# Performance work log

Measured on AMD Instinct MI355X. Metric: run time of the kernel, lower is better.

## Reference

```python
import jax, jax.numpy as jnp
import numpy as np

N = 4096
IN_F = 128
OUT_F = 128
H = 4
D = OUT_F // H  # head_out = 32
SLOPE = 0.2
LN_EPS = 1e-5


def setup_inputs() -> dict:
    key = jax.random.key(0)
    k_x, k_adj, k_W, k_a = jax.random.split(key, 4)
    x = jax.random.normal(k_x, (N, IN_F), dtype=jnp.float32)
    adjacency = jax.random.randint(k_adj, (N, N), 0, 2).astype(jnp.bool_)
    # xavier-uniform-ish init scales
    w_std = float(np.sqrt(2.0 / (IN_F + H * D)))
    a_std = float(np.sqrt(2.0 / (H + 2 * D)))
    W = jax.random.normal(k_W, (H * D, IN_F), dtype=jnp.float32) * w_std  # torch Linear weight layout
    a = jax.random.normal(k_a, (H, 2 * D), dtype=jnp.float32) * a_std
    ln_gamma = jnp.ones((OUT_F,), dtype=jnp.float32)
    ln_beta = jnp.zeros((OUT_F,), dtype=jnp.float32)
    return {"x": x, "adjacency": adjacency, "W": W, "a": a,
            "ln_gamma": ln_gamma, "ln_beta": ln_beta}


def reference(x, adjacency, W, a, ln_gamma, ln_beta):
    # Wx: (N, H, D)
    Wx = (x @ W.T).reshape(N, H, D)
    # e[i,j,h] = leaky_relu( <Wx[i,h], a[h,:D]> + <Wx[j,h], a[h,D:]> )
    # (exact factorization of the original cat([Wx_i, Wx_j]) * a sum)
    alpha_i = jnp.einsum('nhd,hd->nh', Wx, a[:, :D])  # source/i term
    alpha_j = jnp.einsum('nhd,hd->nh', Wx, a[:, D:])  # neighbor/j term
    e = alpha_i[:, None, :] + alpha_j[None, :, :]      # (N, N, H)
    e = jnp.where(e >= 0, e, SLOPE * e)                # LeakyReLU
    e = jnp.where(adjacency[:, :, None], e, -jnp.inf)  # mask non-edges
    attn = jax.nn.softmax(e, axis=1)                   # softmax over j
    out = jnp.einsum('ijh,jhd->ihd', attn, Wx).reshape(N, H * D)
    y = out + x                                        # residual (dims match)
    mu = jnp.mean(y, axis=-1, keepdims=True)
    var = jnp.mean((y - mu) ** 2, axis=-1, keepdims=True)
    return ln_gamma * (y - mu) / jnp.sqrt(var + LN_EPS) + ln_beta
```

## Files before the change

### kernel.cpp

```cpp
#include <hip/hip_runtime.h>
#include <hip/hip_bf16.h>
#include <stdint.h>

#define NN 4096
#define SLOPE 0.2f
#define LOG2E 1.44269504088896340736f

typedef float f32x4 __attribute__((ext_vector_type(4)));
typedef short s16x8 __attribute__((ext_vector_type(8)));
typedef unsigned u32x4 __attribute__((ext_vector_type(4)));

static __device__ __forceinline__ unsigned f32_to_bf16_rne(float f) {
    unsigned u = __builtin_bit_cast(unsigned, f);
    return (u + 0x7FFFu + ((u >> 16) & 1u)) >> 16;
}

__global__ __launch_bounds__(256) void k01(const unsigned* __restrict__ adj_raw,
                                           const float* __restrict__ x,
                                           const float* __restrict__ W,
                                           const float* __restrict__ a,
                                           unsigned* __restrict__ bits,
                                           unsigned* __restrict__ wxb8,
                                           float* __restrict__ ai_s,
                                           float* __restrict__ ajT_s) {
    const int t = threadIdx.x;
    if (blockIdx.x < 2048) {
        __shared__ int s_i32;
        if (t == 0) {
            int all_small = 1;
            for (int i = 0; i < 32; ++i) all_small &= (adj_raw[i] <= 1u);
            s_i32 = all_small;
        }
        __syncthreads();
        const long o = (long)blockIdx.x * 256 + t;
        unsigned mm = 0;
        if (s_i32) {
            const u32x4* p = (const u32x4*)adj_raw + o * 8;
            #pragma unroll
            for (int g = 0; g < 8; ++g) {
                u32x4 v = p[g];
                mm |= (v.x & 1u) << (g * 4) | (v.y & 1u) << (g * 4 + 1) |
                      (v.z & 1u) << (g * 4 + 2) | (v.w & 1u) << (g * 4 + 3);
            }
        } else {
            const u32x4* p = (const u32x4*)adj_raw + o * 2;
            #pragma unroll
            for (int g = 0; g < 2; ++g) {
                u32x4 v = p[g];
                unsigned d[4] = {v.x, v.y, v.z, v.w};
                #pragma unroll
                for (int qq = 0; qq < 4; ++qq)
                    #pragma unroll
                    for (int b = 0; b < 4; ++b)
                        mm |= ((d[qq] >> (8 * b)) & 1u) << (g * 16 + qq * 4 + b);
            }
        }
        bits[o] = mm;
        return;
    }

    __shared__ unsigned short WL[128 * 136];
    __shared__ unsigned short XL[16 * 136];
    __shared__ float WxF[16 * 132];

    const int bid = blockIdx.x - 2048;
    const int i0 = bid * 16;

    for (int p4 = t; p4 < 4096; p4 += 256) {
        f32x4 w4 = *(const f32x4*)(W + 4 * p4);
        unsigned lo = f32_to_bf16_rne(w4.x) | (f32_to_bf16_rne(w4.y) << 16);
        unsigned hi = f32_to_bf16_rne(w4.z) | (f32_to_bf16_rne(w4.w) << 16);
        int c = (4 * p4) >> 7, k = (4 * p4) & 127;
        *(unsigned long long*)&WL[c * 136 + k] =
            (unsigned long long)lo | ((unsigned long long)hi << 32);
    }
    for (int p4 = t; p4 < 512; p4 += 256) {
        f32x4 x4 = *(const f32x4*)(x + (long)i0 * 128 + 4 * p4);
        unsigned lo = f32_to_bf16_rne(x4.x) | (f32_to_bf16_rne(x4.y) << 16);
        unsigned hi = f32_to_bf16_rne(x4.z) | (f32_to_bf16_rne(x4.w) << 16);
        int r = (4 * p4) >> 7, k = (4 * p4) & 127;
        *(unsigned long long*)&XL[r * 136 + k] =
            (unsigned long long)lo | ((unsigned long long)hi << 32);
    }
    __syncthreads();

    const int w = t >> 6, l = t & 63, m = l & 15, q = l >> 4;
    f32x4 acc0 = {0.f, 0.f, 0.f, 0.f}, acc1 = {0.f, 0.f, 0.f, 0.f};
    #pragma unroll
    for (int ks = 0; ks < 4; ++ks) {
        s16x8 af = *(const s16x8*)&XL[m * 136 + ks * 32 + q * 8];
        s16x8 b0 = *(const s16x8*)&WL[(w * 32 + m) * 136 + ks * 32 + q * 8];
        s16x8 b1 = *(const s16x8*)&WL[(w * 32 + 16 + m) * 136 + ks * 32 + q * 8];
        acc0 = __builtin_amdgcn_mfma_f32_16x16x32_bf16(af, b0, acc0, 0, 0, 0);
        acc1 = __builtin_amdgcn_mfma_f32_16x16x32_bf16(af, b1, acc1, 0, 0, 0);
    }
    const int jblk = i0 >> 5;
    const int qp = ((i0 & 16) + q * 4) >> 3;
    const int ehalf = q & 1;
    #pragma unroll
    for (int j2 = 0; j2 < 2; ++j2) {
        f32x4 acc = j2 ? acc1 : acc0;
        unsigned u = (unsigned)__builtin_amdgcn_cvt_pk_fp8_f32(acc[0], acc[1], 0, false);
        u = (unsigned)__builtin_amdgcn_cvt_pk_fp8_f32(acc[2], acc[3], (int)u, true);
        wxb8[(((jblk * 4 + w) * 64 + qp * 16 + m) << 2) + j2 * 2 + ehalf] = u;
        #pragma unroll
        for (int reg = 0; reg < 4; ++reg)
            WxF[(q * 4 + reg) * 132 + (2 * w + j2) * 16 + m] = acc[reg];
    }
    __syncthreads();
    if (t < 64) {
        int r = t >> 2, h = t & 3;
        float s_i = 0.f, s_j = 0.f;
        const float* ar = a + h * 64;
        #pragma unroll
        for (int d = 0; d < 32; ++d) {
            float wv = WxF[r * 132 + h * 32 + d];
            s_i += wv * ar[d];
            s_j += wv * ar[32 + d];
        }
        ai_s[(i0 + r) * 4 + h] = s_i * LOG2E;
        ajT_s[h * NN + i0 + r] = s_j * LOG2E;
    }
}

__global__ __launch_bounds__(1024, 4) void k2_attn(
        const float* __restrict__ x,
        const unsigned* __restrict__ adjbits,
        const unsigned* __restrict__ wxb8,
        const float* __restrict__ ai_s,
        const float* __restrict__ ajT_s,
        const float* __restrict__ gamma,
        const float* __restrict__ beta,
        float* __restrict__ out) {
    __shared__ float ajL[4][4096];
    __shared__ unsigned maskL[16][132];
    __shared__ float C_lds[4][16][32];
    __shared__ float l_lds[4][16];

    const int t = threadIdx.x;
    const int i0 = blockIdx.x * 16;
    const int w = t >> 6, l = t & 63;
    const int h = w & 3, p = w >> 2;
    const int m = l & 15, q = l >> 4;

    {
        const f32x4* src = (const f32x4*)ajT_s;
        f32x4* dst = (f32x4*)&ajL[0][0];
        #pragma unroll
        for (int g = 0; g < 4; ++g) dst[t + 1024 * g] = src[t + 1024 * g];
    }
    {
        #pragma unroll
        for (int g = 0; g < 2; ++g) {
            int idx = t + 1024 * g;
            int r = idx >> 7, c = idx & 127;
            maskL[r][c] = adjbits[(long)(i0 + r) * 128 + c];
        }
    }
    const float ai = ai_s[(i0 + m) * 4 + h];
    __syncthreads();

    const unsigned* bp8 = wxb8 + ((h * 64 + l) << 2);
    const float* ajh = &ajL[h][0] + q * 8;
    const long ONESB = 0x3838383838383838L;

    f32x4 acc0 = {0.f, 0.f, 0.f, 0.f}, acc1 = {0.f, 0.f, 0.f, 0.f};
    f32x4 accl = {0.f, 0.f, 0.f, 0.f};

    u32x4 bv0 = *(const u32x4*)(bp8 + (p << 10));
    u32x4 bv1 = *(const u32x4*)(bp8 + (((p + 4 < 128) ? p + 4 : p) << 10));
    for (int ks = p; ks < 128; ks += 4) {
        const int ksn2 = (ks + 8 < 128) ? (ks + 8) : ks;
        u32x4 bv2 = *(const u32x4*)(bp8 + (ksn2 << 10));

        unsigned mq = (maskL[m][ks] >> (q * 8)) & 0xffu;
        f32x4 aj0 = *(const f32x4*)(ajh + ks * 32);
        f32x4 aj1 = *(const f32x4*)(ajh + ks * 32 + 4);

        float ev[8];
        #pragma unroll
        for (int e = 0; e < 8; ++e) {
            float s = ai + (e < 4 ? aj0[e] : aj1[e - 4]);
            s = fmaxf(s, SLOPE * s);
            float ex = __builtin_amdgcn_exp2f(s);
            ev[e] = ((mq >> e) & 1u) ? ex : 0.0f;
        }
        unsigned d0 = (unsigned)__builtin_amdgcn_cvt_pk_bf8_f32(ev[0], ev[1], 0, false);
        d0 = (unsigned)__builtin_amdgcn_cvt_pk_bf8_f32(ev[2], ev[3], (int)d0, true);
        unsigned d1 = (unsigned)__builtin_amdgcn_cvt_pk_bf8_f32(ev[4], ev[5], 0, false);
        d1 = (unsigned)__builtin_amdgcn_cvt_pk_bf8_f32(ev[6], ev[7], (int)d1, true);
        long av = (long)(((unsigned long long)d1 << 32) | d0);
        long b0 = (long)(((unsigned long long)bv0.y << 32) | bv0.x);
        long b1 = (long)(((unsigned long long)bv0.w << 32) | bv0.z);

        acc0 = __builtin_amdgcn_mfma_f32_16x16x32_bf8_fp8(av, b0, acc0, 0, 0, 0);
        acc1 = __builtin_amdgcn_mfma_f32_16x16x32_bf8_fp8(av, b1, acc1, 0, 0, 0);
        accl = __builtin_amdgcn_mfma_f32_16x16x32_bf8_fp8(av, ONESB, accl, 0, 0, 0);
        bv0 = bv1; bv1 = bv2;
    }

    if (p == 0) {
        #pragma unroll
        for (int reg = 0; reg < 4; ++reg) {
            C_lds[h][q * 4 + reg][m] = acc0[reg];
            C_lds[h][q * 4 + reg][16 + m] = acc1[reg];
            if (m == 0) l_lds[h][q * 4 + reg] = accl[reg];
        }
    }
    __syncthreads();
    if (p == 1) {
        #pragma unroll
        for (int reg = 0; reg < 4; ++reg) {
            C_lds[h][q * 4 + reg][m] += acc0[reg];
            C_lds[h][q * 4 + reg][16 + m] += acc1[reg];
            if (m == 0) l_lds[h][q * 4 + reg] += accl[reg];
        }
    }
    __syncthreads();
    if (p == 2) {
        #pragma unroll
        for (int reg = 0; reg < 4; ++reg) {
            C_lds[h][q * 4 + reg][m] += acc0[reg];
            C_lds[h][q * 4 + reg][16 + m] += acc1[reg];
            if (m == 0) l_lds[h][q * 4 + reg] += accl[reg];
        }
    }
    __syncthreads();
    if (p == 3) {
        #pragma unroll
        for (int reg = 0; reg < 4; ++reg) {
            C_lds[h][q * 4 + reg][m] += acc0[reg];
            C_lds[h][q * 4 + reg][16 + m] += acc1[reg];
            if (m == 0) l_lds[h][q * 4 + reg] += accl[reg];
        }
    }
    __syncthreads();

    if (t < 512) {
        const int r = t >> 5, c32 = t & 31;
        const int f0 = c32 * 4;
        const int hh = f0 >> 5, cl = f0 & 31;
        const float linv = 1.0f / l_lds[hh][r];
        f32x4 xv = *(const f32x4*)(x + (long)(i0 + r) * 128 + f0);
        float y[4], s1 = 0.f, s2 = 0.f;
        #pragma unroll
        for (int kk = 0; kk < 4; ++kk) {
            float yy = C_lds[hh][r][cl + kk] * linv + xv[kk];
            y[kk] = yy; s1 += yy; s2 += yy * yy;
        }
        #pragma unroll
        for (int s = 1; s <= 16; s <<= 1) {
            s1 += __shfl_xor(s1, s, 64);
            s2 += __shfl_xor(s2, s, 64);
        }
        const float mean = s1 * (1.0f / 128.0f);
        const float var = s2 * (1.0f / 128.0f) - mean * mean;
        const float rstd = rsqrtf(var + 1e-5f);
        f32x4 gv = *(const f32x4*)(gamma + f0);
        f32x4 bv2 = *(const f32x4*)(beta + f0);
        f32x4 ov;
        #pragma unroll
        for (int kk = 0; kk < 4; ++kk)
            ov[kk] = gv[kk] * ((y[kk] - mean) * rstd) + bv2[kk];
        *(f32x4*)(out + (long)(i0 + r) * 128 + f0) = ov;
    }
}

extern "C" void kernel_launch(void* const* d_in, const int* in_sizes, int n_in,
                              void* d_out, int out_size, void* d_ws, size_t ws_size,
                              hipStream_t stream) {
    const float* x = (const float*)d_in[0];
    const unsigned* adj_raw = (const unsigned*)d_in[1];
    const float* W = (const float*)d_in[2];
    const float* a = (const float*)d_in[3];
    const float* gamma = (const float*)d_in[4];
    const float* beta = (const float*)d_in[5];

    unsigned* wxb8 = (unsigned*)d_ws;
    float* ai_s = (float*)((char*)d_ws + (512 << 10));
    float* ajT_s = (float*)((char*)d_ws + (576 << 10));
    unsigned* adjbits = (unsigned*)((char*)d_ws + (1 << 20));

    k01<<<2304, 256, 0, stream>>>(adj_raw, x, W, a, adjbits, wxb8, ai_s, ajT_s);
    k2_attn<<<256, 1024, 0, stream>>>(x, adjbits, wxb8, ai_s, ajT_s, gamma, beta,
                                      (float*)d_out);
}
```

Before: 132.0 us.

## Fuse adjacency bit-packing into attention kernel, drop packed-mask round trip

Moves the conversion of the raw boolean/int adjacency into per-row bitmasks from the first kernel into the attention kernel, where each block packs its own 16 rows straight into shared memory. The first kernel now only computes Wx and the attention logits, with 256 blocks instead of 2304. This removes the write and re-read of the packed mask buffer through global memory and the extra blocks in the first launch. In exchange, the attention kernel's prologue reads the full raw adjacency rows before its main loop, which lengthens the critical path of the 256 large blocks, and there is less parallelism available to stream that data.

After: 134.1 us. No clear change (+1.6%).

```diff
diff --git a/kernel.cpp b/kernel.cpp
--- a/kernel.cpp
+++ b/kernel.cpp
@@ -15,56 +15,18 @@
     return (u + 0x7FFFu + ((u >> 16) & 1u)) >> 16;
 }
 
-__global__ __launch_bounds__(256) void k01(const unsigned* __restrict__ adj_raw,
-                                           const float* __restrict__ x,
-                                           const float* __restrict__ W,
-                                           const float* __restrict__ a,
-                                           unsigned* __restrict__ bits,
-                                           unsigned* __restrict__ wxb8,
-                                           float* __restrict__ ai_s,
-                                           float* __restrict__ ajT_s) {
-    const int t = threadIdx.x;
-    if (blockIdx.x < 2048) {
-        __shared__ int s_i32;
-        if (t == 0) {
-            int all_small = 1;
-            for (int i = 0; i < 32; ++i) all_small &= (adj_raw[i] <= 1u);
-            s_i32 = all_small;
-        }
-        __syncthreads();
-        const long o = (long)blockIdx.x * 256 + t;
-        unsigned mm = 0;
-        if (s_i32) {
-            const u32x4* p = (const u32x4*)adj_raw + o * 8;
-            #pragma unroll
-            for (int g = 0; g < 8; ++g) {
-                u32x4 v = p[g];
-                mm |= (v.x & 1u) << (g * 4) | (v.y & 1u) << (g * 4 + 1) |
-                      (v.z & 1u) << (g * 4 + 2) | (v.w & 1u) << (g * 4 + 3);
-            }
-        } else {
-            const u32x4* p = (const u32x4*)adj_raw + o * 2;
-            #pragma unroll
-            for (int g = 0; g < 2; ++g) {
-                u32x4 v = p[g];
-                unsigned d[4] = {v.x, v.y, v.z, v.w};
-                #pragma unroll
-                for (int qq = 0; qq < 4; ++qq)
-                    #pragma unroll
-                    for (int b = 0; b < 4; ++b)
-                        mm |= ((d[qq] >> (8 * b)) & 1u) << (g * 16 + qq * 4 + b);
-            }
-        }
-        bits[o] = mm;
-        return;
-    }
-
+__global__ __launch_bounds__(256) void k1_wx(const float* __restrict__ x,
+                                             const float* __restrict__ W,
+                                             const float* __restrict__ a,
+                                             unsigned* __restrict__ wxb8,
+                                             float* __restrict__ ai_s,
+                                             float* __restrict__ ajT_s) {
     __shared__ unsigned short WL[128 * 136];
     __shared__ unsigned short XL[16 * 136];
     __shared__ float WxF[16 * 132];
 
-    const int bid = blockIdx.x - 2048;
-    const int i0 = bid * 16;
+    const int t = threadIdx.x;
+    const int i0 = blockIdx.x * 16;
 
     for (int p4 = t; p4 < 4096; p4 += 256) {
         f32x4 w4 = *(const f32x4*)(W + 4 * p4);
@@ -125,7 +87,7 @@
 
 __global__ __launch_bounds__(1024, 4) void k2_attn(
         const float* __restrict__ x,
-        const unsigned* __restrict__ adjbits,
+        const unsigned* __restrict__ adj_raw,
         const unsigned* __restrict__ wxb8,
         const float* __restrict__ ai_s,
         const float* __restrict__ ajT_s,
@@ -142,6 +104,10 @@
     const int w = t >> 6, l = t & 63;
     const int h = w & 3, p = w >> 2;
     const int m = l & 15, q = l >> 4;
+    const int rt = t >> 6, ct = t & 63;
+
+    unsigned dv = adj_raw[l & 31];
+    const bool is_i32 = __all(dv <= 1u) != 0;
 
     {
         const f32x4* src = (const f32x4*)ajT_s;
@@ -150,11 +116,33 @@
         for (int g = 0; g < 4; ++g) dst[t + 1024 * g] = src[t + 1024 * g];
     }
     {
-        #pragma unroll
-        for (int g = 0; g < 2; ++g) {
-            int idx = t + 1024 * g;
-            int r = idx >> 7, c = idx & 127;
-            maskL[r][c] = adjbits[(long)(i0 + r) * 128 + c];
+        unsigned short* mh = (unsigned short*)&maskL[0][0];
+        if (is_i32) {
+            #pragma unroll
+            for (int c = 0; c < 4; ++c) {
+                const u32x4* ps = (const u32x4*)(adj_raw + (long)(i0 + rt) * NN +
+                                                 c * 1024 + ct * 16);
+                u32x4 r0 = ps[0], r1 = ps[1], r2 = ps[2], r3 = ps[3];
+                unsigned b =
+                    (r0.x & 1u) | ((r0.y & 1u) << 1) | ((r0.z & 1u) << 2) | ((r0.w & 1u) << 3) |
+                    ((r1.x & 1u) << 4) | ((r1.y & 1u) << 5) | ((r1.z & 1u) << 6) | ((r1.w & 1u) << 7) |
+                    ((r2.x & 1u) << 8) | ((r2.y & 1u) << 9) | ((r2.z & 1u) << 10) | ((r2.w & 1u) << 11) |
+                    ((r3.x & 1u) << 12) | ((r3.y & 1u) << 13) | ((r3.z & 1u) << 14) | ((r3.w & 1u) << 15);
+                mh[(rt * 132 + c * 32 + (ct >> 1)) * 2 + (ct & 1)] = (unsigned short)b;
+            }
+        } else {
+            #pragma unroll
+            for (int c = 0; c < 4; ++c) {
+                const u32x4* ps = (const u32x4*)((const unsigned char*)adj_raw +
+                                                 (long)(i0 + rt) * NN + c * 1024 + ct * 16);
+                u32x4 r0 = ps[0];
+                unsigned n0 = (((r0.x & 0x01010101u) * 0x08040201u) >> 24) & 0xFu;
+                unsigned n1 = (((r0.y & 0x01010101u) * 0x08040201u) >> 24) & 0xFu;
+                unsigned n2 = (((r0.z & 0x01010101u) * 0x08040201u) >> 24) & 0xFu;
+                unsigned n3 = (((r0.w & 0x01010101u) * 0x08040201u) >> 24) & 0xFu;
+                unsigned b = n0 | (n1 << 4) | (n2 << 8) | (n3 << 12);
+                mh[(rt * 132 + c * 32 + (ct >> 1)) * 2 + (ct & 1)] = (unsigned short)b;
+            }
         }
     }
     const float ai = ai_s[(i0 + m) * 4 + h];
@@ -279,9 +267,8 @@
     unsigned* wxb8 = (unsigned*)d_ws;
     float* ai_s = (float*)((char*)d_ws + (512 << 10));
     float* ajT_s = (float*)((char*)d_ws + (576 << 10));
-    unsigned* adjbits = (unsigned*)((char*)d_ws + (1 << 20));
-
-    k01<<<2304, 256, 0, stream>>>(adj_raw, x, W, a, adjbits, wxb8, ai_s, ajT_s);
-    k2_attn<<<256, 1024, 0, stream>>>(x, adjbits, wxb8, ai_s, ajT_s, gamma, beta,
+
+    k1_wx<<<256, 256, 0, stream>>>(x, W, a, wxb8, ai_s, ajT_s);
+    k2_attn<<<256, 1024, 0, stream>>>(x, adj_raw, wxb8, ai_s, ajT_s, gamma, beta,
                                       (float*)d_out);
 }
```

## Factor exp of leaky-relu into per-node exponentials and switch attention MFMA to fp16

Applied to the files above, without the earlier changes.

Uses exp2(leaky(ai+aj)) = max(exp2(ai)exp2(aj), exp2(.2ai)exp2(.2aj)) to precompute per-node exponentials in the first kernel. The inner attention loop then replaces eight transcendental exp2 calls per step with packed fp16 multiplies and a max. Wx and the attention weights move from fp8/bf8 to fp16, with the MFMA changing from bf8_fp8 to f16. This doubles the Wx bytes streamed per step and carries a risk of fp16 overflow or underflow in the products, since nothing subtracts a running max.

After: 129.4 us, median of 2. 2.0% less time.

```diff
diff --git a/kernel.cpp b/kernel.cpp
--- a/kernel.cpp
+++ b/kernel.cpp
@@ -1,18 +1,21 @@
 #include <hip/hip_runtime.h>
-#include <hip/hip_bf16.h>
 #include <stdint.h>
 
 #define NN 4096
-#define SLOPE 0.2f
 #define LOG2E 1.44269504088896340736f
 
 typedef float f32x4 __attribute__((ext_vector_type(4)));
 typedef short s16x8 __attribute__((ext_vector_type(8)));
 typedef unsigned u32x4 __attribute__((ext_vector_type(4)));
+typedef _Float16 f16x2 __attribute__((ext_vector_type(2)));
 
 static __device__ __forceinline__ unsigned f32_to_bf16_rne(float f) {
     unsigned u = __builtin_bit_cast(unsigned, f);
     return (u + 0x7FFFu + ((u >> 16) & 1u)) >> 16;
+}
+static __device__ __forceinline__ unsigned f16bits(float f) {
+    _Float16 h = (_Float16)f;
+    return (unsigned)__builtin_bit_cast(unsigned short, h);
 }
 
 __global__ __launch_bounds__(256) void k01(const unsigned* __restrict__ adj_raw,
@@ -20,9 +23,9 @@
                                            const float* __restrict__ W,
                                            const float* __restrict__ a,
                                            unsigned* __restrict__ bits,
-                                           unsigned* __restrict__ wxb8,
+                                           unsigned* __restrict__ wxb16,
                                            float* __restrict__ ai_s,
-                                           float* __restrict__ ajT_s) {
+                                           unsigned* __restrict__ ejfj) {
     const int t = threadIdx.x;
     if (blockIdx.x < 2048) {
         __shared__ int s_i32;
@@ -95,17 +98,20 @@
         acc1 = __builtin_amdgcn_mfma_f32_16x16x32_bf16(af, b1, acc1, 0, 0, 0);
     }
     const int jblk = i0 >> 5;
-    const int qp = ((i0 & 16) + q * 4) >> 3;
-    const int ehalf = q & 1;
+    const int qslot = ((i0 & 16) + q * 4) >> 3;
+    const int dhalf = q & 1;
     #pragma unroll
     for (int j2 = 0; j2 < 2; ++j2) {
+        const int fblk = 2 * w + j2;
         f32x4 acc = j2 ? acc1 : acc0;
-        unsigned u = (unsigned)__builtin_amdgcn_cvt_pk_fp8_f32(acc[0], acc[1], 0, false);
-        u = (unsigned)__builtin_amdgcn_cvt_pk_fp8_f32(acc[2], acc[3], (int)u, true);
-        wxb8[(((jblk * 4 + w) * 64 + qp * 16 + m) << 2) + j2 * 2 + ehalf] = u;
+        unsigned d01 = f16bits(acc[0]) | (f16bits(acc[1]) << 16);
+        unsigned d23 = f16bits(acc[2]) | (f16bits(acc[3]) << 16);
+        unsigned* wp = wxb16 + (((jblk * 8 + fblk) * 64 + qslot * 16 + m) << 2) + dhalf * 2;
+        wp[0] = d01;
+        wp[1] = d23;
         #pragma unroll
         for (int reg = 0; reg < 4; ++reg)
-            WxF[(q * 4 + reg) * 132 + (2 * w + j2) * 16 + m] = acc[reg];
+            WxF[(q * 4 + reg) * 132 + fblk * 16 + m] = acc[reg];
     }
     __syncthreads();
     if (t < 64) {
@@ -119,20 +125,21 @@
             s_j += wv * ar[32 + d];
         }
         ai_s[(i0 + r) * 4 + h] = s_i * LOG2E;
-        ajT_s[h * NN + i0 + r] = s_j * LOG2E;
+        float sjl = s_j * LOG2E;
+        ejfj[h * NN + i0 + r] = f16bits(exp2f(sjl)) | (f16bits(exp2f(0.2f * sjl)) << 16);
     }
 }
 
 __global__ __launch_bounds__(1024, 4) void k2_attn(
         const float* __restrict__ x,
         const unsigned* __restrict__ adjbits,
-        const unsigned* __restrict__ wxb8,
+        const unsigned* __restrict__ wxb16,
         const float* __restrict__ ai_s,
-        const float* __restrict__ ajT_s,
+        const unsigned* __restrict__ ejfj,
         const float* __restrict__ gamma,
         const float* __restrict__ beta,
         float* __restrict__ out) {
-    __shared__ float ajL[4][4096];
+    __shared__ unsigned efL[4][4096];
     __shared__ unsigned maskL[16][132];
     __shared__ float C_lds[4][16][32];
     __shared__ float l_lds[4][16];
@@ -144,8 +151,8 @@
     const int m = l & 15, q = l >> 4;
 
     {
-        const f32x4* src = (const f32x4*)ajT_s;
-        f32x4* dst = (f32x4*)&ajL[0][0];
+        const u32x4* src = (const u32x4*)ejfj;
+        u32x4* dst = (u32x4*)&efL[0][0];
         #pragma unroll
         for (int g = 0; g < 4; ++g) dst[t + 1024 * g] = src[t + 1024 * g];
     }
@@ -157,46 +164,57 @@
             maskL[r][c] = adjbits[(long)(i0 + r) * 128 + c];
         }
     }
-    const float ai = ai_s[(i0 + m) * 4 + h];
-    __syncthreads();
-
-    const unsigned* bp8 = wxb8 + ((h * 64 + l) << 2);
-    const float* ajh = &ajL[h][0] + q * 8;
-    const long ONESB = 0x3838383838383838L;
+    const float aif = ai_s[(i0 + m) * 4 + h];
+    const _Float16 eiH = (_Float16)exp2f(aif);
+    const _Float16 fiH = (_Float16)exp2f(0.2f * aif);
+    const f16x2 Ei2 = {eiH, eiH};
+    const f16x2 Fi2 = {fiH, fiH};
+    __syncthreads();
+
+    const unsigned* bp16 = wxb16 + ((2 * h) * 64 + l) * 4;
+    const unsigned* efh = &efL[h][0] + q * 8;
+    const s16x8 ONESH = {0x3C00, 0x3C00, 0x3C00, 0x3C00,
+                         0x3C00, 0x3C00, 0x3C00, 0x3C00};
 
     f32x4 acc0 = {0.f, 0.f, 0.f, 0.f}, acc1 = {0.f, 0.f, 0.f, 0.f};
     f32x4 accl = {0.f, 0.f, 0.f, 0.f};
 
-    u32x4 bv0 = *(const u32x4*)(bp8 + (p << 10));
-    u32x4 bv1 = *(const u32x4*)(bp8 + (((p + 4 < 128) ? p + 4 : p) << 10));
+    const int ks1 = (p + 4 < 128) ? p + 4 : p;
+    u32x4 pa0 = *(const u32x4*)(bp16 + p * 2048);
+    u32x4 pb0 = *(const u32x4*)(bp16 + p * 2048 + 256);
+    u32x4 pa1 = *(const u32x4*)(bp16 + ks1 * 2048);
+    u32x4 pb1 = *(const u32x4*)(bp16 + ks1 * 2048 + 256);
+
     for (int ks = p; ks < 128; ks += 4) {
         const int ksn2 = (ks + 8 < 128) ? (ks + 8) : ks;
-        u32x4 bv2 = *(const u32x4*)(bp8 + (ksn2 << 10));
+        u32x4 pa2 = *(const u32x4*)(bp16 + ksn2 * 2048);
+        u32x4 pb2 = *(const u32x4*)(bp16 + ksn2 * 2048 + 256);
 
         unsigned mq = (maskL[m][ks] >> (q * 8)) & 0xffu;
-        f32x4 aj0 = *(const f32x4*)(ajh + ks * 32);
-        f32x4 aj1 = *(const f32x4*)(ajh + ks * 32 + 4);
-
-        float ev[8];
-        #pragma unroll
-        for (int e = 0; e < 8; ++e) {
-            float s = ai + (e < 4 ? aj0[e] : aj1[e - 4]);
-            s = fmaxf(s, SLOPE * s);
-            float ex = __builtin_amdgcn_exp2f(s);
-            ev[e] = ((mq >> e) & 1u) ? ex : 0.0f;
-        }
-        unsigned d0 = (unsigned)__builtin_amdgcn_cvt_pk_bf8_f32(ev[0], ev[1], 0, false);
-        d0 = (unsigned)__builtin_amdgcn_cvt_pk_bf8_f32(ev[2], ev[3], (int)d0, true);
-        unsigned d1 = (unsigned)__builtin_amdgcn_cvt_pk_bf8_f32(ev[4], ev[5], 0, false);
-        d1 = (unsigned)__builtin_amdgcn_cvt_pk_bf8_f32(ev[6], ev[7], (int)d1, true);
-        long av = (long)(((unsigned long long)d1 << 32) | d0);
-        long b0 = (long)(((unsigned long long)bv0.y << 32) | bv0.x);
-        long b1 = (long)(((unsigned long long)bv0.w << 32) | bv0.z);
-
-        acc0 = __builtin_amdgcn_mfma_f32_16x16x32_bf8_fp8(av, b0, acc0, 0, 0, 0);
-        acc1 = __builtin_amdgcn_mfma_f32_16x16x32_bf8_fp8(av, b1, acc1, 0, 0, 0);
-        accl = __builtin_amdgcn_mfma_f32_16x16x32_bf8_fp8(av, ONESB, accl, 0, 0, 0);
-        bv0 = bv1; bv1 = bv2;
+        u32x4 ef0 = *(const u32x4*)(efh + ks * 32);
+        u32x4 ef1 = *(const u32x4*)(efh + ks * 32 + 4);
+        unsigned efu[8] = {ef0.x, ef0.y, ef0.z, ef0.w, ef1.x, ef1.y, ef1.z, ef1.w};
+
+        union { s16x8 v; unsigned u[4]; } af;
+        #pragma unroll
+        for (int pr = 0; pr < 4; ++pr) {
+            unsigned d0 = efu[2 * pr], d1 = efu[2 * pr + 1];
+            unsigned Ep = __builtin_amdgcn_perm(d1, d0, 0x05040100);
+            unsigned Fp = __builtin_amdgcn_perm(d1, d0, 0x07060302);
+            f16x2 mE = Ei2 * __builtin_bit_cast(f16x2, Ep);
+            f16x2 mF = Fi2 * __builtin_bit_cast(f16x2, Fp);
+            f16x2 mx = __builtin_elementwise_max(mE, mF);
+            unsigned lo = (unsigned)(-(int)((mq >> (2 * pr)) & 1u));
+            unsigned hi = (unsigned)(-(int)((mq >> (2 * pr + 1)) & 1u));
+            unsigned msk = (lo & 0xFFFFu) | (hi & 0xFFFF0000u);
+            af.u[pr] = __builtin_bit_cast(unsigned, mx) & msk;
+        }
+        union { u32x4 u; s16x8 s; } b0c, b1c;
+        b0c.u = pa0; b1c.u = pb0;
+        acc0 = __builtin_amdgcn_mfma_f32_16x16x32_f16(af.v, b0c.s, acc0, 0, 0, 0);
+        acc1 = __builtin_amdgcn_mfma_f32_16x16x32_f16(af.v, b1c.s, acc1, 0, 0, 0);
+        accl = __builtin_amdgcn_mfma_f32_16x16x32_f16(af.v, ONESH, accl, 0, 0, 0);
+        pa0 = pa1; pb0 = pb1; pa1 = pa2; pb1 = pb2;
     }
 
     if (p == 0) {
@@ -257,11 +275,11 @@
         const float var = s2 * (1.0f / 128.0f) - mean * mean;
         const float rstd = rsqrtf(var + 1e-5f);
         f32x4 gv = *(const f32x4*)(gamma + f0);
-        f32x4 bv2 = *(const f32x4*)(beta + f0);
+        f32x4 bv = *(const f32x4*)(beta + f0);
         f32x4 ov;
         #pragma unroll
         for (int kk = 0; kk < 4; ++kk)
-            ov[kk] = gv[kk] * ((y[kk] - mean) * rstd) + bv2[kk];
+            ov[kk] = gv[kk] * ((y[kk] - mean) * rstd) + bv[kk];
         *(f32x4*)(out + (long)(i0 + r) * 128 + f0) = ov;
     }
 }
@@ -276,12 +294,12 @@
     const float* gamma = (const float*)d_in[4];
     const float* beta = (const float*)d_in[5];
 
-    unsigned* wxb8 = (unsigned*)d_ws;
-    float* ai_s = (float*)((char*)d_ws + (512 << 10));
-    float* ajT_s = (float*)((char*)d_ws + (576 << 10));
-    unsigned* adjbits = (unsigned*)((char*)d_ws + (1 << 20));
-
-    k01<<<2304, 256, 0, stream>>>(adj_raw, x, W, a, adjbits, wxb8, ai_s, ajT_s);
-    k2_attn<<<256, 1024, 0, stream>>>(x, adjbits, wxb8, ai_s, ajT_s, gamma, beta,
+    unsigned* wxb16 = (unsigned*)d_ws;
+    float* ai_s = (float*)((char*)d_ws + (1 << 20));
+    unsigned* ejfj = (unsigned*)((char*)d_ws + (1 << 20) + (64 << 10));
+    unsigned* adjbits = (unsigned*)((char*)d_ws + (2 << 20));
+
+    k01<<<2304, 256, 0, stream>>>(adj_raw, x, W, a, adjbits, wxb16, ai_s, ejfj);
+    k2_attn<<<256, 1024, 0, stream>>>(x, adjbits, wxb16, ai_s, ejfj, gamma, beta,
                                       (float*)d_out);
 }
```
